# Kernel tuning notes

Measured on AMD Instinct MI355X. Metric: run time of the kernel, lower is better.

Reference implementation:

```python
import jax, jax.numpy as jnp
import numpy as np

B_SZ, L, H, P = 16, 1024, 256, 256
DT_MIN, DT_MAX = 1e-3, 1e-1


def setup_inputs() -> dict:
    key = jax.random.key(0)
    ks = jax.random.split(key, 6)
    u = jax.random.normal(ks[0], (B_SZ, L, H), dtype=jnp.float32)
    # Stable diagonal init (stands in for HiPPO-LegS diag: negative real part,
    # spread imaginary parts) so exp(Lambda*Delta) has |.|<1 over long scans.
    Lambda_re = -0.5 * jnp.ones((P,), jnp.float32)
    Lambda_im = jnp.pi * jnp.arange(P, dtype=jnp.float32)
    Bp = jax.random.normal(ks[1], (P, H, 2), jnp.float32) / jnp.sqrt(2.0 * H)  # (P,H,2) real/imag
    Cp = jax.random.normal(ks[2], (H, P, 2), jnp.float32) / jnp.sqrt(2.0 * P)  # (H,P,2) real/imag
    D = jax.random.normal(ks[3], (H,), jnp.float32)
    log_step = (jax.random.uniform(ks[4], (P, 1), jnp.float32)
                * (jnp.log(DT_MAX) - jnp.log(DT_MIN)) + jnp.log(DT_MIN))
    return {"u": u, "Lambda_re": Lambda_re, "Lambda_im": Lambda_im,
            "B": Bp, "C": Cp, "D": D, "log_step": log_step}


def _binop(ei, ej):
    # S5 associative scan element: (A, Bu); compose linear recurrences.
    ai, bi = ei
    aj, bj = ej
    return aj * ai, aj * bi + bj


def reference(u, Lambda_re, Lambda_im, B, C, D, log_step):
    # clip_eigs=False, step_rescale=1.0, conj_sym=True, discretization='zoh'
    Lambda = Lambda_re + 1j * Lambda_im                     # (P,) complex
    B_tilde = B[..., 0] + 1j * B[..., 1]                    # (P,H) complex
    C_tilde = C[..., 0] + 1j * C[..., 1]                    # (H,P) complex
    Delta = jnp.exp(log_step[:, 0])                         # (P,)
    # ZOH discretization
    Lambda_bar = jnp.exp(Lambda * Delta)                    # (P,)
    B_bar = ((Lambda_bar - 1.0) / Lambda)[:, None] * B_tilde  # (P,H)
    # Input projection: (B, L, P) complex
    Bu = jnp.einsum('ph,blh->blp', B_bar, u.astype(B_bar.dtype))
    Lam = jnp.broadcast_to(Lambda_bar, Bu.shape)            # (B, L, P)
    # Parallel associative scan over time axis
    _, xs = jax.lax.associative_scan(_binop, (Lam, Bu), axis=1)  # states (B,L,P)
    # Output projection; conj_sym -> 2 * real part
    ys = 2.0 * jnp.einsum('hp,blp->blh', C_tilde, xs).real  # (B,L,H)
    return ys + D * u                                       # feedthrough
```

## Files before the change

kernel.cpp:

```cpp
#include <hip/hip_runtime.h>
#include <hip/hip_bf16.h>
#include <math.h>

#define BB     16
#define LSEQ   1024
#define HH     256
#define PP     256
#define LC     32
#define NC     (LSEQ/LC)
#define NCHUNK (BB*NC)

#define OFF_W1T  0u
#define OFF_W2T  262144u
#define OFF_PW   524288u
#define OFF_CEND 655360u
#define OFF_BAR  2752512u

typedef __attribute__((ext_vector_type(8))) short short8;
typedef __attribute__((ext_vector_type(4))) float floatx4;
typedef unsigned long long ull;

__device__ __forceinline__ float bf2f(unsigned hs) {
    union { unsigned u; float f; } v; v.u = hs << 16; return v.f;
}
__device__ __forceinline__ unsigned short f2bs(float f) {
    __hip_bfloat16 h = __float2bfloat16(f);
    union { __hip_bfloat16 h; unsigned short s; } v; v.h = h; return v.s;
}
__device__ __forceinline__ unsigned packbf(float r, float i) {
    return (unsigned)f2bs(r) | ((unsigned)f2bs(i) << 16);
}
__device__ __forceinline__ void async16(const void* g, void* l) {
    __builtin_amdgcn_global_load_lds(
        (const __attribute__((address_space(1))) unsigned*)g,
        (__attribute__((address_space(3))) unsigned*)l, 16, 0, 0);
}
__device__ __forceinline__ float2 lam_pow(float lr, float li, float dtt) {
    float m = expf(lr * dtt);
    return make_float2(m * cosf(li * dtt), m * sinf(li * dtt));
}
__device__ __forceinline__ void cohst32(unsigned* p, unsigned v) {
    __hip_atomic_store(p, v, __ATOMIC_RELAXED, __HIP_MEMORY_SCOPE_AGENT);
}
__device__ __forceinline__ void cohst64(ull* p, float2 v) {
    ull b; __builtin_memcpy(&b, &v, 8);
    __hip_atomic_store(p, b, __ATOMIC_RELAXED, __HIP_MEMORY_SCOPE_AGENT);
}

__device__ __forceinline__ void treebar(char* base, int inst) {
    asm volatile("s_waitcnt vmcnt(0)" ::: "memory");
    __syncthreads();
    if (threadIdx.x == 0) {
        char* b = base + inst * 8192;
        const unsigned g = blockIdx.x >> 4;
        unsigned* gcnt  = (unsigned*)(b + g * 64);
        unsigned* gflag = (unsigned*)(b + 2048 + g * 64);
        unsigned* rcnt  = (unsigned*)(b + 4096);
        unsigned* rflag = (unsigned*)(b + 4160);
        unsigned r = __hip_atomic_fetch_add(gcnt, 1u, __ATOMIC_RELAXED,
                                            __HIP_MEMORY_SCOPE_AGENT);
        if (r == 15) {
            unsigned rr = __hip_atomic_fetch_add(rcnt, 1u, __ATOMIC_RELAXED,
                                                 __HIP_MEMORY_SCOPE_AGENT);
            if (rr == 31) {
                __hip_atomic_store(rflag, 1u, __ATOMIC_RELAXED, __HIP_MEMORY_SCOPE_AGENT);
            } else {
                for (int it = 0; it < (1 << 18); ++it) {
                    if (__hip_atomic_load(rflag, __ATOMIC_RELAXED, __HIP_MEMORY_SCOPE_AGENT))
                        break;
                    __builtin_amdgcn_s_sleep(4);
                }
            }
            __hip_atomic_store(gflag, 1u, __ATOMIC_RELAXED, __HIP_MEMORY_SCOPE_AGENT);
        } else {
            for (int it = 0; it < (1 << 18); ++it) {
                if (__hip_atomic_load(gflag, __ATOMIC_RELAXED, __HIP_MEMORY_SCOPE_AGENT))
                    break;
                __builtin_amdgcn_s_sleep(4);
            }
        }
    }
    __syncthreads();
}

#define XSTRS 520
#define XSTRD 260
#define BSB2_OFF 34816
#define CARR_OFF 67584

__global__ __launch_bounds__(512, 4) void k_all(
        const float* __restrict__ u, const float* __restrict__ Lr,
        const float* __restrict__ Li, const float* __restrict__ ls,
        const float* __restrict__ Bm, const float* __restrict__ Cm,
        const float* __restrict__ D, float* __restrict__ out,
        char* __restrict__ ws) {
    extern __shared__ char smem[];
    char* barbase = ws + OFF_BAR;

    const int tid = threadIdx.x, bc = blockIdx.x;
    const int wave = tid >> 6, lane = tid & 63;
    const int q = lane >> 4, rr = lane & 15;
    const int c4 = lane & 3, r4 = lane >> 2;
    const int m0 = bc * LC;

    if (bc < 256) {
        if (tid < 128) {
            int p = bc, t = tid;
            float lr = Lr[p], li = Li[p];
            float dt = expf(ls[p]);
            float2 lam = lam_pow(lr, li, dt);
            float den = lr * lr + li * li;
            float nr = lam.x - 1.0f, ni = lam.y;
            float cr = (nr * lr + ni * li) / den;
            float ci = (ni * lr - nr * li) / den;
            float4 bv = *(const float4*)(Bm + (size_t)p * 512 + 4 * t);
            unsigned rev = packbf(cr * bv.x - ci * bv.y, cr * bv.z - ci * bv.w);
            unsigned imv = packbf(cr * bv.y + ci * bv.x, cr * bv.w + ci * bv.z);
            unsigned* w1u = (unsigned*)(ws + OFF_W1T);
            cohst32(&w1u[(2 * p) * 128 + t], rev);
            cohst32(&w1u[(2 * p + 1) * 128 + t], imv);
            if (t <= 32)
                cohst64((ull*)(ws + OFF_PW) + (size_t)t * 256 + p,
                        lam_pow(lr, li, dt * (float)t));
        }
    } else {
        if (tid < 256) {
            int h = bc - 256, p = tid;
            float c_r = Cm[(h * PP + p) * 2 + 0];
            float c_i = Cm[(h * PP + p) * 2 + 1];
            cohst32((unsigned*)(ws + OFF_W2T) + h * 256 + p, packbf(2.0f * c_r, -2.0f * c_i));
        }
    }
    treebar(barbase, 0);

    {
        char* Asb = smem;
        char* Bsb = smem + 4096;
        const unsigned short* W1 = (const unsigned short*)(ws + OFF_W1T);
        floatx4 acc[2][4];
        #pragma unroll
        for (int i = 0; i < 2; ++i)
            #pragma unroll
            for (int j = 0; j < 4; ++j) acc[i][j] = (floatx4)0.0f;

        const int arow = tid >> 4, acol4 = (tid & 15) * 4;
        for (int k0 = 0; k0 < 256; k0 += 64) {
            __syncthreads();
            {
                float4 v = *(const float4*)(u + (size_t)(m0 + arow) * 256 + k0 + acol4);
                *(uint2*)(Asb + (acol4 >> 5) * 2048 + arow * 64 + (acol4 & 31) * 2) =
                    make_uint2(packbf(v.x, v.y), packbf(v.z, v.w));
            }
            #pragma unroll
            for (int t = 0; t < 8; ++t) {
                int idx = t * 8 + wave;
                int pan = idx & 1, rowg = idx >> 1;
                int row = rowg * 16 + r4;
                async16(W1 + (size_t)row * 256 + k0 + pan * 32 + c4 * 8,
                        Bsb + pan * 32768 + row * 64 + c4 * 16);
            }
            __syncthreads();
            #pragma unroll
            for (int ks = 0; ks < 2; ++ks) {
                short8 a0 = *(const short8*)(Asb + ks * 2048 + rr * 64 + q * 16);
                short8 a1 = *(const short8*)(Asb + ks * 2048 + (16 + rr) * 64 + q * 16);
                #pragma unroll
                for (int j = 0; j < 4; ++j) {
                    short8 b = *(const short8*)(Bsb + ks * 32768 +
                                                (wave * 64 + j * 16 + rr) * 64 + q * 16);
                    acc[0][j] = __builtin_amdgcn_mfma_f32_16x16x32_bf16(a0, b, acc[0][j], 0, 0, 0);
                    acc[1][j] = __builtin_amdgcn_mfma_f32_16x16x32_bf16(a1, b, acc[1][j], 0, 0, 0);
                }
            }
        }
        __syncthreads();
        unsigned short* X = (unsigned short*)smem;
        #pragma unroll
        for (int i = 0; i < 2; ++i)
            #pragma unroll
            for (int j = 0; j < 4; ++j)
                #pragma unroll
                for (int r0 = 0; r0 < 4; ++r0)
                    X[(i * 16 + q * 4 + r0) * XSTRS + wave * 64 + j * 16 + rr] =
                        f2bs(acc[i][j][r0]);
        __syncthreads();
    }

    if (tid < 256) {
        const int pq = tid;
        const float2 lam = lam_pow(Lr[pq], Li[pq], expf(ls[pq]));
        unsigned* X32 = (unsigned*)smem;
        float xr = 0.0f, xi = 0.0f;
        #pragma unroll
        for (int j = 0; j < LC; ++j) {
            unsigned cv = X32[j * XSTRD + pq];
            float br = bf2f(cv & 0xffffu), bi = bf2f(cv >> 16);
            float nr = fmaf(lam.x, xr, fmaf(-lam.y, xi, br));
            float ni = fmaf(lam.x, xi, fmaf(lam.y, xr, bi));
            xr = nr; xi = ni;
            X32[j * XSTRD + pq] = packbf(xr, xi);
        }
        cohst64((ull*)(ws + OFF_CEND) + (size_t)bc * 256 + pq, make_float2(xr, xi));
    } else {
        const unsigned short* W2 = (const unsigned short*)(ws + OFF_W2T);
        char* Bsb2 = smem + BSB2_OFF;
        int w4 = wave - 4;
        #pragma unroll
        for (int t = 0; t < 8; ++t) {
            int idx = t * 4 + w4;
            int pan = idx & 1, rowg = idx >> 1;
            int row = rowg * 16 + r4;
            async16(W2 + (size_t)row * 512 + pan * 32 + c4 * 8,
                    Bsb2 + pan * 16384 + row * 64 + c4 * 16);
        }
    }
    treebar(barbase, 1);

    {
        float2* carrs = (float2*)(smem + CARR_OFF);
        if (tid < 256) {
            const int p = tid;
            const int c = bc & (NC - 1);
            const int b0 = bc & ~(NC - 1);
            const float2* cend = (const float2*)(ws + OFF_CEND);
            const float2 g = lam_pow(Lr[p], Li[p], expf(ls[p]) * (float)LC);
            float sr = 0.0f, si = 0.0f;
            float gpr = 1.0f, gpi = 0.0f;
            #pragma unroll
            for (int k = 0; k < NC - 1; ++k) {
                int idx = c - 1 - k; idx = idx < 0 ? 0 : idx;
                float2 e = cend[(size_t)(b0 + idx) * 256 + p];
                float er = (k < c) ? e.x : 0.0f;
                float ei = (k < c) ? e.y : 0.0f;
                sr = fmaf(gpr, er, fmaf(-gpi, ei, sr));
                si = fmaf(gpr, ei, fmaf(gpi, er, si));
                float t2 = gpr * g.x - gpi * g.y;
                gpi = gpr * g.y + gpi * g.x; gpr = t2;
            }
            carrs[p] = make_float2(sr, si);
        }
        __syncthreads();
    }

    {
        float2* carrs = (float2*)(smem + CARR_OFF);
        unsigned* X32 = (unsigned*)smem;
        const float2* pw = (const float2*)(ws + OFF_PW);
        const int frow = tid >> 4, fcol = tid & 15;
        const float2* pwr = pw + (size_t)(frow + 1) * 256;
        #pragma unroll 4
        for (int e = 0; e < 16; ++e) {
            int p = fcol + e * 16;
            unsigned cv = X32[frow * XSTRD + p];
            float2 pwv = pwr[p];
            float2 cav = carrs[p];
            float fr = pwv.x * cav.x - pwv.y * cav.y;
            float fi = pwv.x * cav.y + pwv.y * cav.x;
            X32[frow * XSTRD + p] =
                packbf(bf2f(cv & 0xffffu) + fr, bf2f(cv >> 16) + fi);
        }
    }

    {
        const unsigned short* W2 = (const unsigned short*)(ws + OFF_W2T);
        char* Bsb2 = smem + BSB2_OFF;
        const char* Xb = (const char*)smem;
        floatx4 acc[2][2];
        #pragma unroll
        for (int i = 0; i < 2; ++i)
            #pragma unroll
            for (int j = 0; j < 2; ++j) acc[i][j] = (floatx4)0.0f;

        for (int k0 = 0; k0 < 512; k0 += 64) {
            if (k0) {
                __syncthreads();
                #pragma unroll
                for (int t = 0; t < 4; ++t) {
                    int idx = t * 8 + wave;
                    int pan = idx & 1, rowg = idx >> 1;
                    int row = rowg * 16 + r4;
                    async16(W2 + (size_t)row * 512 + k0 + pan * 32 + c4 * 8,
                            Bsb2 + pan * 16384 + row * 64 + c4 * 16);
                }
            }
            __syncthreads();
            #pragma unroll
            for (int ks = 0; ks < 2; ++ks) {
                short8 a[2], bfr[2];
                #pragma unroll
                for (int i = 0; i < 2; ++i)
                    a[i] = *(const short8*)(Xb + (i * 16 + rr) * (XSTRS * 2) +
                                            k0 * 2 + ks * 64 + q * 16);
                #pragma unroll
                for (int j = 0; j < 2; ++j)
                    bfr[j] = *(const short8*)(Bsb2 + ks * 16384 +
                                              (wave * 32 + j * 16 + rr) * 64 + q * 16);
                #pragma unroll
                for (int i = 0; i < 2; ++i)
                    #pragma unroll
                    for (int j = 0; j < 2; ++j)
                        acc[i][j] = __builtin_amdgcn_mfma_f32_16x16x32_bf16(a[i], bfr[j], acc[i][j], 0, 0, 0);
            }
        }

        #pragma unroll
        for (int i = 0; i < 2; ++i) {
            int mbase = m0 + i * 16 + q * 4;
            #pragma unroll
            for (int j = 0; j < 2; ++j) {
                int col = wave * 32 + j * 16 + rr;
                #pragma unroll
                for (int r0 = 0; r0 < 4; ++r0) {
                    int rw = mbase + r0;
                    size_t gi = (size_t)rw * 256 + col;
                    out[gi] = acc[i][j][r0] + D[col] * u[gi];
                }
            }
        }
    }
}

extern "C" void kernel_launch(void* const* d_in, const int* in_sizes, int n_in,
                              void* d_out, int out_size, void* d_ws, size_t ws_size,
                              hipStream_t stream) {
    const float* u  = (const float*)d_in[0];
    const float* Lr = (const float*)d_in[1];
    const float* Li = (const float*)d_in[2];
    const float* Bm = (const float*)d_in[3];
    const float* Cm = (const float*)d_in[4];
    const float* D  = (const float*)d_in[5];
    const float* ls = (const float*)d_in[6];
    float* out = (float*)d_out;
    char* ws = (char*)d_ws;

    hipMemsetAsync(ws + OFF_BAR, 0, 16384, stream);
    k_all<<<NCHUNK, 512, 69632, stream>>>(u, Lr, Li, ls, Bm, Cm, D, out, ws);
}
```

Baseline: 109.9 us.

## Load GEMM weights directly from global memory and prefetch u before barrier

Both projection GEMMs now read their B-operand fragments straight from global/L2 instead of staging them through LDS with async loads and per-k-step barriers. The whole 32x256 u tile is loaded before the first grid barrier and stored once into a swizzled LDS layout, which removes the k-loop syncs. LDS use roughly halves, which could allow more resident blocks. The cost is uncoalesced 16-byte global reads per lane on the critical MFMA path, which relies on the weights being L2-resident.

Result: slower. 124.5 us (+13.2%).

```diff
diff --git a/kernel.cpp b/kernel.cpp
--- a/kernel.cpp
+++ b/kernel.cpp
@@ -29,11 +29,6 @@
 }
 __device__ __forceinline__ unsigned packbf(float r, float i) {
     return (unsigned)f2bs(r) | ((unsigned)f2bs(i) << 16);
-}
-__device__ __forceinline__ void async16(const void* g, void* l) {
-    __builtin_amdgcn_global_load_lds(
-        (const __attribute__((address_space(1))) unsigned*)g,
-        (__attribute__((address_space(3))) unsigned*)l, 16, 0, 0);
 }
 __device__ __forceinline__ float2 lam_pow(float lr, float li, float dtt) {
     float m = expf(lr * dtt);
@@ -85,8 +80,7 @@
 
 #define XSTRS 520
 #define XSTRD 260
-#define BSB2_OFF 34816
-#define CARR_OFF 67584
+#define CARR_OFF 33280
 
 __global__ __launch_bounds__(512, 4) void k_all(
         const float* __restrict__ u, const float* __restrict__ Lr,
@@ -100,8 +94,15 @@
     const int tid = threadIdx.x, bc = blockIdx.x;
     const int wave = tid >> 6, lane = tid & 63;
     const int q = lane >> 4, rr = lane & 15;
-    const int c4 = lane & 3, r4 = lane >> 2;
     const int m0 = bc * LC;
+
+    const int arow = tid >> 4, acol = (tid & 15) * 16;
+    float4 uv[4];
+    {
+        const float* up = u + (size_t)(m0 + arow) * 256 + acol;
+        #pragma unroll
+        for (int i = 0; i < 4; ++i) uv[i] = *(const float4*)(up + 4 * i);
+    }
 
     if (bc < 256) {
         if (tid < 128) {
@@ -131,46 +132,42 @@
             cohst32((unsigned*)(ws + OFF_W2T) + h * 256 + p, packbf(2.0f * c_r, -2.0f * c_i));
         }
     }
+
+    {
+        unsigned pk[8];
+        #pragma unroll
+        for (int i = 0; i < 4; ++i) {
+            pk[2 * i]     = packbf(uv[i].x, uv[i].y);
+            pk[2 * i + 1] = packbf(uv[i].z, uv[i].w);
+        }
+        const int kb = acol * 2;
+        const int msk = (arow & 7) << 4;
+        char* A = smem;
+        *(uint4*)(A + arow * 512 + (kb ^ msk))        = make_uint4(pk[0], pk[1], pk[2], pk[3]);
+        *(uint4*)(A + arow * 512 + ((kb + 16) ^ msk)) = make_uint4(pk[4], pk[5], pk[6], pk[7]);
+    }
     treebar(barbase, 0);
 
     {
-        char* Asb = smem;
-        char* Bsb = smem + 4096;
-        const unsigned short* W1 = (const unsigned short*)(ws + OFF_W1T);
+        const char* W1 = (const char*)(ws + OFF_W1T);
+        const char* A = smem;
+        const int amask = (rr & 7) << 4;
         floatx4 acc[2][4];
         #pragma unroll
         for (int i = 0; i < 2; ++i)
             #pragma unroll
             for (int j = 0; j < 4; ++j) acc[i][j] = (floatx4)0.0f;
 
-        const int arow = tid >> 4, acol4 = (tid & 15) * 4;
-        for (int k0 = 0; k0 < 256; k0 += 64) {
-            __syncthreads();
-            {
-                float4 v = *(const float4*)(u + (size_t)(m0 + arow) * 256 + k0 + acol4);
-                *(uint2*)(Asb + (acol4 >> 5) * 2048 + arow * 64 + (acol4 & 31) * 2) =
-                    make_uint2(packbf(v.x, v.y), packbf(v.z, v.w));
-            }
-            #pragma unroll
-            for (int t = 0; t < 8; ++t) {
-                int idx = t * 8 + wave;
-                int pan = idx & 1, rowg = idx >> 1;
-                int row = rowg * 16 + r4;
-                async16(W1 + (size_t)row * 256 + k0 + pan * 32 + c4 * 8,
-                        Bsb + pan * 32768 + row * 64 + c4 * 16);
-            }
-            __syncthreads();
-            #pragma unroll
-            for (int ks = 0; ks < 2; ++ks) {
-                short8 a0 = *(const short8*)(Asb + ks * 2048 + rr * 64 + q * 16);
-                short8 a1 = *(const short8*)(Asb + ks * 2048 + (16 + rr) * 64 + q * 16);
-                #pragma unroll
-                for (int j = 0; j < 4; ++j) {
-                    short8 b = *(const short8*)(Bsb + ks * 32768 +
-                                                (wave * 64 + j * 16 + rr) * 64 + q * 16);
-                    acc[0][j] = __builtin_amdgcn_mfma_f32_16x16x32_bf16(a0, b, acc[0][j], 0, 0, 0);
-                    acc[1][j] = __builtin_amdgcn_mfma_f32_16x16x32_bf16(a1, b, acc[1][j], 0, 0, 0);
-                }
+        #pragma unroll 2
+        for (int hs = 0; hs < 8; ++hs) {
+            const int kb = hs * 64 + q * 16;
+            short8 a0 = *(const short8*)(A + rr * 512 + (kb ^ amask));
+            short8 a1 = *(const short8*)(A + (16 + rr) * 512 + (kb ^ amask));
+            #pragma unroll
+            for (int j = 0; j < 4; ++j) {
+                short8 b = *(const short8*)(W1 + (size_t)(wave * 64 + j * 16 + rr) * 512 + kb);
+                acc[0][j] = __builtin_amdgcn_mfma_f32_16x16x32_bf16(a0, b, acc[0][j], 0, 0, 0);
+                acc[1][j] = __builtin_amdgcn_mfma_f32_16x16x32_bf16(a1, b, acc[1][j], 0, 0, 0);
             }
         }
         __syncthreads();
@@ -201,18 +198,6 @@
             X32[j * XSTRD + pq] = packbf(xr, xi);
         }
         cohst64((ull*)(ws + OFF_CEND) + (size_t)bc * 256 + pq, make_float2(xr, xi));
-    } else {
-        const unsigned short* W2 = (const unsigned short*)(ws + OFF_W2T);
-        char* Bsb2 = smem + BSB2_OFF;
-        int w4 = wave - 4;
-        #pragma unroll
-        for (int t = 0; t < 8; ++t) {
-            int idx = t * 4 + w4;
-            int pan = idx & 1, rowg = idx >> 1;
-            int row = rowg * 16 + r4;
-            async16(W2 + (size_t)row * 512 + pan * 32 + c4 * 8,
-                    Bsb2 + pan * 16384 + row * 64 + c4 * 16);
-        }
     }
     treebar(barbase, 1);
 
@@ -259,11 +244,11 @@
             X32[frow * XSTRD + p] =
                 packbf(bf2f(cv & 0xffffu) + fr, bf2f(cv >> 16) + fi);
         }
-    }
-
-    {
-        const unsigned short* W2 = (const unsigned short*)(ws + OFF_W2T);
-        char* Bsb2 = smem + BSB2_OFF;
+        __syncthreads();
+    }
+
+    {
+        const char* W2 = (const char*)(ws + OFF_W2T);
         const char* Xb = (const char*)smem;
         floatx4 acc[2][2];
         #pragma unroll
@@ -271,36 +256,21 @@
             #pragma unroll
             for (int j = 0; j < 2; ++j) acc[i][j] = (floatx4)0.0f;
 
-        for (int k0 = 0; k0 < 512; k0 += 64) {
-            if (k0) {
-                __syncthreads();
-                #pragma unroll
-                for (int t = 0; t < 4; ++t) {
-                    int idx = t * 8 + wave;
-                    int pan = idx & 1, rowg = idx >> 1;
-                    int row = rowg * 16 + r4;
-                    async16(W2 + (size_t)row * 512 + k0 + pan * 32 + c4 * 8,
-                            Bsb2 + pan * 16384 + row * 64 + c4 * 16);
-                }
-            }
-            __syncthreads();
-            #pragma unroll
-            for (int ks = 0; ks < 2; ++ks) {
-                short8 a[2], bfr[2];
-                #pragma unroll
-                for (int i = 0; i < 2; ++i)
-                    a[i] = *(const short8*)(Xb + (i * 16 + rr) * (XSTRS * 2) +
-                                            k0 * 2 + ks * 64 + q * 16);
+        #pragma unroll 2
+        for (int hs = 0; hs < 16; ++hs) {
+            const int kb = hs * 64 + q * 16;
+            short8 a[2], bfr[2];
+            #pragma unroll
+            for (int i = 0; i < 2; ++i)
+                a[i] = *(const short8*)(Xb + (i * 16 + rr) * (XSTRS * 2) + kb);
+            #pragma unroll
+            for (int j = 0; j < 2; ++j)
+                bfr[j] = *(const short8*)(W2 + (size_t)(wave * 32 + j * 16 + rr) * 1024 + kb);
+            #pragma unroll
+            for (int i = 0; i < 2; ++i)
                 #pragma unroll
                 for (int j = 0; j < 2; ++j)
-                    bfr[j] = *(const short8*)(Bsb2 + ks * 16384 +
-                                              (wave * 32 + j * 16 + rr) * 64 + q * 16);
-                #pragma unroll
-                for (int i = 0; i < 2; ++i)
-                    #pragma unroll
-                    for (int j = 0; j < 2; ++j)
-                        acc[i][j] = __builtin_amdgcn_mfma_f32_16x16x32_bf16(a[i], bfr[j], acc[i][j], 0, 0, 0);
-            }
+                    acc[i][j] = __builtin_amdgcn_mfma_f32_16x16x32_bf16(a[i], bfr[j], acc[i][j], 0, 0, 0);
         }
 
         #pragma unroll
@@ -334,5 +304,5 @@
     char* ws = (char*)d_ws;
 
     hipMemsetAsync(ws + OFF_BAR, 0, 16384, stream);
-    k_all<<<NCHUNK, 512, 69632, stream>>>(u, Lr, Li, ls, Bm, Cm, D, out, ws);
-}
+    k_all<<<NCHUNK, 512, 35328, stream>>>(u, Lr, Li, ls, Bm, Cm, D, out, ws);
+}
```
